# Optimization experiments

Hardware: AMD Instinct MI355X
Metric: run time of the kernel (lower is better)

Reference implementation:

```python
import jax, jax.numpy as jnp
import numpy as np

MU = 2.0 ** -10  # sign-LMS weight adaptation step


def setup_inputs() -> dict:
    key = jax.random.key(0)
    # 16-bit-range hyperspectral cube [Z, Y, X]
    image = jax.random.normal(key, (202, 256, 256), dtype=jnp.float32) * 1000.0
    # adaptive predictor weights per band over P=3 previous bands, init 0
    w0 = jnp.zeros((202, 3), dtype=jnp.float32)
    return {"image": image, "w0": w0}


def reference(image, w0):
    Z, Y, X = image.shape
    P = w0.shape[1]
    max_val = 2.0 ** 15 - 1.0  # dynamic_range = 16
    min_val = -(2.0 ** 15)

    # Spectral neighborhood: previous P bands at the same (y, x), zero-padded.
    # (lossless mode => sample representatives == original samples, so
    #  cross-band dependence uses raw samples directly)
    nb = jnp.stack(
        [jnp.pad(image, ((p + 1, 0), (0, 0), (0, 0)))[:Z] for p in range(P)],
        axis=-1,
    )  # [Z, Y, X, P]

    s_flat = image.reshape(Z, Y * X)       # BSQ raster order within each band
    nb_flat = nb.reshape(Z, Y * X, P)

    def band_scan(w_init, s_z, nb_z):
        # Sequential adaptive prediction within one band (strict data dependency)
        def step(w, inp):
            s, n = inp
            pred = jnp.clip(jnp.dot(w, n), min_val, max_val)
            res = s - pred
            w_new = w + MU * jnp.sign(res) * n  # sign-LMS update
            return w_new, (pred, res)

        _, (preds, ress) = jax.lax.scan(step, w_init, (s_z, nb_z))
        return preds, ress

    preds, ress = jax.vmap(band_scan)(w0, s_flat, nb_flat)  # bands independent
    predictions = preds.reshape(Z, Y, X)
    residuals = ress.reshape(Z, Y, X)

    # Lossless: quantized residual == residual; map rounded residual to
    # non-negative index delta = 2q (q>=0) or -2q-1 (q<0)
    q = jnp.round(residuals).astype(jnp.int32)
    mapped_indices = jnp.where(q >= 0, 2 * q, -2 * q - 1)
    quantized_residuals = residuals
    sample_representatives = image
    reconstructed = predictions + quantized_residuals

    return (predictions, residuals, quantized_residuals, mapped_indices,
            sample_representatives, reconstructed)
```

## Files before the change

kernel.cpp:

```cpp
#include <hip/hip_runtime.h>

#define ZB 202
#define ZBP 208
#define YX 65536
#define NTOT ((size_t)ZB * YX)

#define SS 128
#define NSS (YX / SS)
#define PAD 4

__device__ __forceinline__ constexpr float kMU() { return 0.0009765625f; }
#define MINV (-32768.0f)
#define MAXV (32767.0f)

typedef float v2f __attribute__((ext_vector_type(2)));

#define GL_LDS4(g, l)                                                     \
    __builtin_amdgcn_global_load_lds(                                     \
        (const __attribute__((address_space(1))) void*)(g),               \
        (__attribute__((address_space(3))) void*)(l), 4, 0, 0)

__global__ __launch_bounds__(256) void tr_kernel(const float* __restrict__ img,
                                                 float* __restrict__ imgT) {
    __shared__ float lds[64 * 65];
    const int t0 = blockIdx.x * 64;
    const int zi = blockIdx.y;
    const int zw0 = zi * 64 - 3;
    const int tid = threadIdx.x;
    const int c = tid & 63;
    const int r0 = tid >> 6;

    for (int k = 0; k < 16; ++k) {
        int rr = r0 * 16 + k;
        int z = zw0 + rr;
        float v = 0.0f;
        if (z >= 0 && z < ZB) v = img[(size_t)z * YX + t0 + c];
        lds[rr * 65 + c] = v;
    }
    __syncthreads();

    const int l = tid & 63;
    const int off = zi * 64 + l;
    if (off < ZBP) {
        for (int k = 0; k < 16; ++k) {
            int tr = r0 * 16 + k;
            imgT[(size_t)(t0 + tr) * ZBP + off] = lds[l * 65 + tr];
        }
    }
}

__global__ __launch_bounds__(512, 1) void scan_kernel(const float* __restrict__ imgT,
                                                      const float* __restrict__ w0g,
                                                      float* __restrict__ dT) {
    __shared__ float ldsf[PAD + 2 * SS * 64];

    const int tid = threadIdx.x;
    const int lane = tid & 63;
    const int wv = tid >> 6;
    const int b = blockIdx.x;
    const int goff = 61 * b + lane;
    const float* gsrc = imgT + goff;

    const int band = 61 * b + lane - 3;
    const bool live = (lane >= 3) && (band < ZB);
    const int wband = band < 0 ? 0 : (band > ZB - 1 ? ZB - 1 : band);
    float w0 = w0g[wband * 3 + 0];
    float w1 = w0g[wband * 3 + 1];
    float w2 = w0g[wband * 3 + 2];
    float* const sbase = live ? (dT + band) : (dT + NTOT + 70 + lane);

    auto stage = [&](int st) {
        float* lp = ldsf + PAD + (st & 1) * (SS * 64);
        const float* gp = gsrc + (size_t)st * (SS * ZBP);
        for (int r = wv - 1; r < SS; r += 7)
            GL_LDS4(gp + (size_t)r * ZBP, lp + r * 64);
    };

    v2f Aa[16], Ab[16], Ba[16], Bb[16];

#define RTISSUE(XA, XB, bsel, st_)                                             \
    {                                                                          \
        uint32_t a0_ = (uint32_t)(size_t)(__attribute__((address_space(3)))    \
            float*)(ldsf + (PAD + (bsel) * (SS * 64) + (st_) * (16 * 64)       \
                            + lane - 3));                                      \
        _Pragma("unroll") for (int k = 0; k < 16; ++k) {                       \
            uint32_t a_ = a0_ + (uint32_t)(k * 256);                           \
            asm volatile("ds_read2_b32 %0, %2 offset0:0 offset1:1\n\t"         \
                         "ds_read2_b32 %1, %2 offset0:2 offset1:3"             \
                         : "=&v"(XA[k]), "=&v"(XB[k])                          \
                         : "v"(a_));                                           \
        }                                                                      \
    }

#define KWAIT()                                                                \
    {                                                                          \
        asm volatile("s_waitcnt lgkmcnt(0)" ::: "memory");                     \
        __builtin_amdgcn_sched_barrier(0);                                     \
    }

#define CP(BA, BB, st_)                                                        \
    {                                                                          \
        float* op = sbase + ((size_t)ss * SS + (st_) * 16) * ZB;               \
        _Pragma("unroll") for (int i = 0; i < 16; ++i) {                       \
            const float nx = BA[i].x, ny = BA[i].y;                            \
            const float nz = BB[i].x, s_ = BB[i].y;                            \
            float d = __fadd_rn(                                               \
                __fadd_rn(__fmul_rn(w0, nz), __fmul_rn(w1, ny)),               \
                __fmul_rn(w2, nx));                                            \
            float sg = (s_ > d) ? kMU() : ((s_ < d) ? -kMU() : 0.0f);          \
            w0 = __builtin_fmaf(sg, nz, w0);                                   \
            w1 = __builtin_fmaf(sg, ny, w1);                                   \
            w2 = __builtin_fmaf(sg, nx, w2);                                   \
            op[(size_t)i * ZB] = d;                                            \
        }                                                                      \
    }

    if (wv != 0) stage(0);
    __syncthreads();

    for (int ss = 0; ss < NSS; ++ss) {
        if (wv != 0) {
            if (ss + 1 < NSS) stage(ss + 1);
        } else {
            const int csel = ss & 1;
            RTISSUE(Aa, Ab, csel, 0); KWAIT();
            RTISSUE(Ba, Bb, csel, 1); CP(Aa, Ab, 0); KWAIT();
            RTISSUE(Aa, Ab, csel, 2); CP(Ba, Bb, 1); KWAIT();
            RTISSUE(Ba, Bb, csel, 3); CP(Aa, Ab, 2); KWAIT();
            RTISSUE(Aa, Ab, csel, 4); CP(Ba, Bb, 3); KWAIT();
            RTISSUE(Ba, Bb, csel, 5); CP(Aa, Ab, 4); KWAIT();
            RTISSUE(Aa, Ab, csel, 6); CP(Ba, Bb, 5); KWAIT();
            RTISSUE(Ba, Bb, csel, 7); CP(Aa, Ab, 6); KWAIT();
            CP(Ba, Bb, 7);
        }
        __syncthreads();
    }

#undef RTISSUE
#undef KWAIT
#undef CP
}

__global__ __launch_bounds__(256) void finalize_kernel(const float* __restrict__ img,
                                                       const float* __restrict__ dT,
                                                       float* __restrict__ out) {
    __shared__ float lds[64 * ZB];
    const int t0 = blockIdx.x * 64;
    const float* src = dT + (size_t)t0 * ZB;
    for (int i = threadIdx.x; i < 64 * ZB; i += 256) lds[i] = src[i];
    __syncthreads();

    for (int k = 0; k < 51; ++k) {
        int e = k * 256 + threadIdx.x;
        if (e < 64 * ZB) {
            int zz = e >> 6;
            int tl = e & 63;
            float dv = lds[tl * ZB + zz];
            float pred = fminf(fmaxf(dv, MINV), MAXV);
            size_t o = (size_t)zz * YX + t0 + tl;
            float s = img[o];
            float res = __fsub_rn(s, pred);
            int q = (int)rintf(res);
            int m = (q >= 0) ? (2 * q) : (-2 * q - 1);
            out[o] = pred;
            out[NTOT + o] = res;
            out[2 * NTOT + o] = res;
            out[3 * NTOT + o] = (float)m;
            out[5 * NTOT + o] = __fadd_rn(pred, res);
        }
    }
}

__global__ __launch_bounds__(256) void repr_kernel(const float4* __restrict__ img4,
                                                   float4* __restrict__ out4) {
    size_t n4 = NTOT / 4;
    for (size_t i = (size_t)blockIdx.x * blockDim.x + threadIdx.x; i < n4;
         i += (size_t)gridDim.x * blockDim.x)
        out4[i] = img4[i];
}

extern "C" void kernel_launch(void* const* d_in, const int* in_sizes, int n_in,
                              void* d_out, int out_size, void* d_ws, size_t ws_size,
                              hipStream_t stream) {
    const float* img = (const float*)d_in[0];
    const float* w0g = (const float*)d_in[1];
    float* out = (float*)d_out;

    float* imgT = out;
    float* dT = out + 4 * NTOT;

    tr_kernel<<<dim3(YX / 64, 4), 256, 0, stream>>>(img, imgT);
    scan_kernel<<<4, 512, 0, stream>>>(imgT, w0g, dT);
    finalize_kernel<<<YX / 64, 256, 0, stream>>>(img, dT, out);
    repr_kernel<<<4096, 256, 0, stream>>>((const float4*)img, (float4*)(out + 4 * NTOT));
}
```

Measured before the change: 2.773 ms.

## Fuse transpose, finalize and copy into the scan kernel

The transpose, finalize and representative-copy kernels are removed. The scan kernel now gathers band data straight from the original image into LDS, writes predictions to an LDS output buffer, and its helper waves compute and store all six outputs for the previous chunk while wave 0 scans the current one. This avoids the transposed intermediate round trips through global memory and three extra launches. In exchange, all output traffic is issued by only 4 blocks (28 waves), and the LDS gathers use strided per-band 4-byte loads.

```diff
diff --git a/kernel.cpp b/kernel.cpp
--- a/kernel.cpp
+++ b/kernel.cpp
@@ -1,10 +1,9 @@
 #include <hip/hip_runtime.h>
+#include <stdint.h>
 
 #define ZB 202
-#define ZBP 208
 #define YX 65536
 #define NTOT ((size_t)ZB * YX)
-
 #define SS 128
 #define NSS (YX / SS)
 #define PAD 4
@@ -20,87 +19,115 @@
         (const __attribute__((address_space(1))) void*)(g),               \
         (__attribute__((address_space(3))) void*)(l), 4, 0, 0)
 
-__global__ __launch_bounds__(256) void tr_kernel(const float* __restrict__ img,
-                                                 float* __restrict__ imgT) {
-    __shared__ float lds[64 * 65];
-    const int t0 = blockIdx.x * 64;
-    const int zi = blockIdx.y;
-    const int zw0 = zi * 64 - 3;
-    const int tid = threadIdx.x;
-    const int c = tid & 63;
-    const int r0 = tid >> 6;
-
-    for (int k = 0; k < 16; ++k) {
-        int rr = r0 * 16 + k;
-        int z = zw0 + rr;
-        float v = 0.0f;
-        if (z >= 0 && z < ZB) v = img[(size_t)z * YX + t0 + c];
-        lds[rr * 65 + c] = v;
-    }
-    __syncthreads();
-
-    const int l = tid & 63;
-    const int off = zi * 64 + l;
-    if (off < ZBP) {
-        for (int k = 0; k < 16; ++k) {
-            int tr = r0 * 16 + k;
-            imgT[(size_t)(t0 + tr) * ZBP + off] = lds[l * 65 + tr];
-        }
-    }
-}
-
-__global__ __launch_bounds__(512, 1) void scan_kernel(const float* __restrict__ imgT,
+__global__ __launch_bounds__(512, 1) void scan_kernel(const float* __restrict__ img,
                                                       const float* __restrict__ w0g,
-                                                      float* __restrict__ dT) {
+                                                      float* __restrict__ out) {
     __shared__ float ldsf[PAD + 2 * SS * 64];
+    __shared__ float ldso[2 * SS * 64];
 
     const int tid = threadIdx.x;
     const int lane = tid & 63;
     const int wv = tid >> 6;
     const int b = blockIdx.x;
-    const int goff = 61 * b + lane;
-    const float* gsrc = imgT + goff;
+
+    float* const o_pred = out;
+    float* const o_res  = out + NTOT;
+    float* const o_qres = out + 2 * NTOT;
+    float* const o_map  = out + 3 * NTOT;
+    float* const o_repr = out + 4 * NTOT;
+    float* const o_rec  = out + 5 * NTOT;
 
     const int band = 61 * b + lane - 3;
-    const bool live = (lane >= 3) && (band < ZB);
     const int wband = band < 0 ? 0 : (band > ZB - 1 ? ZB - 1 : band);
     float w0 = w0g[wband * 3 + 0];
     float w1 = w0g[wband * 3 + 1];
     float w2 = w0g[wband * 3 + 2];
-    float* const sbase = live ? (dT + band) : (dT + NTOT + 70 + lane);
+    v2f Aa[16], Ab[16], Ba[16], Bb[16];
+    const uint32_t inb0 =
+        (uint32_t)(size_t)(__attribute__((address_space(3))) float*)(ldsf + PAD + lane - 3);
+    const uint32_t otbC =
+        (uint32_t)(size_t)(__attribute__((address_space(3))) float*)(ldso) + (uint32_t)(lane * 4);
+    const uint32_t otbP =
+        (uint32_t)(size_t)(__attribute__((address_space(3))) float*)(ldso) + (uint32_t)(lane * 256);
+
+    const int zcl = band < 0 ? 0 : (band > ZB - 1 ? ZB - 1 : band);
+    const float* const Bz = img + (size_t)zcl * YX;
+    const int cmax = (204 - 61 * b) < 63 ? (204 - 61 * b) : 63;
+
+    float sA[9], sB[9], dA[9], dB[9];
 
     auto stage = [&](int st) {
-        float* lp = ldsf + PAD + (st & 1) * (SS * 64);
-        const float* gp = gsrc + (size_t)st * (SS * ZBP);
+        float* lp0 = ldsf + PAD + (st & 1) * (SS * 64);
+        const float* p = Bz + (size_t)st * SS;
         for (int r = wv - 1; r < SS; r += 7)
-            GL_LDS4(gp + (size_t)r * ZBP, lp + r * 64);
+            GL_LDS4(p + r, lp0 + r * 64);
+    };
+    auto rezero = [&](int bn) {
+        float* lp0 = ldsf + PAD + bn * (SS * 64);
+        for (int r = wv - 1; r < SS; r += 7) {
+            lp0[r * 64 + 0] = 0.0f; lp0[r * 64 + 1] = 0.0f; lp0[r * 64 + 2] = 0.0f;
+        }
+    };
+    auto pissue = [&](int Tp, uint32_t pbuf) {
+#pragma unroll
+        for (int k = 0; k < 9; ++k) {
+            const int c = 2 + wv + 7 * k;
+            const int cc = c <= cmax ? c : 3;
+            const int zz = 61 * b + cc - 3;
+            const float* sp = img + (size_t)zz * YX + Tp + lane;
+            asm volatile("global_load_dword %0, %2, off\n\t"
+                         "global_load_dword %1, %2, off offset:256"
+                         : "=&v"(sA[k]), "=&v"(sB[k]) : "v"(sp));
+            uint32_t da = otbP + pbuf + (uint32_t)(cc * 4);
+            asm volatile("ds_read_b32 %0, %2\n\t"
+                         "ds_read_b32 %1, %2 offset:16384"
+                         : "=&v"(dA[k]), "=&v"(dB[k]) : "v"(da));
+        }
+    };
+    auto pstore = [&](int Tp) {
+#pragma unroll
+        for (int k = 0; k < 9; ++k) {
+            const int c = 2 + wv + 7 * k;
+            if (c > cmax) continue;
+            const int zz = 61 * b + c - 3;
+            const size_t o = (size_t)zz * YX + Tp + lane;
+#pragma unroll
+            for (int h = 0; h < 2; ++h) {
+                const float dv = h ? dB[k] : dA[k];
+                const float s = h ? sB[k] : sA[k];
+                const size_t oo = o + (size_t)(h * 64);
+                const float pred = fminf(fmaxf(dv, MINV), MAXV);
+                const float res = __fsub_rn(s, pred);
+                const int q = (int)rintf(res);
+                const int m = (q >= 0) ? (2 * q) : (-2 * q - 1);
+                o_pred[oo] = pred;
+                o_res[oo] = res;
+                o_qres[oo] = res;
+                o_map[oo] = (float)m;
+                o_repr[oo] = s;
+                o_rec[oo] = __fadd_rn(pred, res);
+            }
+        }
     };
 
-    v2f Aa[16], Ab[16], Ba[16], Bb[16];
-
-#define RTISSUE(XA, XB, bsel, st_)                                             \
+#define RTISSUE(XA, XB, cb_, st_)                                              \
     {                                                                          \
-        uint32_t a0_ = (uint32_t)(size_t)(__attribute__((address_space(3)))    \
-            float*)(ldsf + (PAD + (bsel) * (SS * 64) + (st_) * (16 * 64)       \
-                            + lane - 3));                                      \
+        uint32_t a0_ = inb0 + (cb_) + (uint32_t)((st_) * 4096);                \
         _Pragma("unroll") for (int k = 0; k < 16; ++k) {                       \
             uint32_t a_ = a0_ + (uint32_t)(k * 256);                           \
             asm volatile("ds_read2_b32 %0, %2 offset0:0 offset1:1\n\t"         \
                          "ds_read2_b32 %1, %2 offset0:2 offset1:3"             \
-                         : "=&v"(XA[k]), "=&v"(XB[k])                          \
-                         : "v"(a_));                                           \
+                         : "=&v"(XA[k]), "=&v"(XB[k]) : "v"(a_));              \
         }                                                                      \
     }
-
 #define KWAIT()                                                                \
     {                                                                          \
         asm volatile("s_waitcnt lgkmcnt(0)" ::: "memory");                     \
         __builtin_amdgcn_sched_barrier(0);                                     \
     }
-
-#define CP(BA, BB, st_)                                                        \
+#define CP(BA, BB, cb_, st_)                                                   \
     {                                                                          \
-        float* op = sbase + ((size_t)ss * SS + (st_) * 16) * ZB;               \
+        uint32_t ob_ = otbC + (cb_) + (uint32_t)((st_) * 4096);                \
         _Pragma("unroll") for (int i = 0; i < 16; ++i) {                       \
             const float nx = BA[i].x, ny = BA[i].y;                            \
             const float nz = BB[i].x, s_ = BB[i].y;                            \
@@ -111,72 +138,51 @@
             w0 = __builtin_fmaf(sg, nz, w0);                                   \
             w1 = __builtin_fmaf(sg, ny, w1);                                   \
             w2 = __builtin_fmaf(sg, nx, w2);                                   \
-            op[(size_t)i * ZB] = d;                                            \
+            asm volatile("ds_write_b32 %0, %1 offset:%c2"                      \
+                         :: "v"(ob_), "v"(d), "i"((i) * 256) : "memory");      \
         }                                                                      \
     }
 
-    if (wv != 0) stage(0);
+    if (wv != 0) {
+        stage(0);
+        asm volatile("s_waitcnt vmcnt(0)" ::: "memory");
+        if (b == 0) rezero(0);
+    }
     __syncthreads();
 
     for (int ss = 0; ss < NSS; ++ss) {
-        if (wv != 0) {
+        if (wv == 0) {
+            const uint32_t cb = (uint32_t)((ss & 1) * 32768);
+            RTISSUE(Aa, Ab, cb, 0); KWAIT();
+            RTISSUE(Ba, Bb, cb, 1); CP(Aa, Ab, cb, 0); KWAIT();
+            RTISSUE(Aa, Ab, cb, 2); CP(Ba, Bb, cb, 1); KWAIT();
+            RTISSUE(Ba, Bb, cb, 3); CP(Aa, Ab, cb, 2); KWAIT();
+            RTISSUE(Aa, Ab, cb, 4); CP(Ba, Bb, cb, 3); KWAIT();
+            RTISSUE(Ba, Bb, cb, 5); CP(Aa, Ab, cb, 4); KWAIT();
+            RTISSUE(Aa, Ab, cb, 6); CP(Ba, Bb, cb, 5); KWAIT();
+            RTISSUE(Ba, Bb, cb, 7); CP(Aa, Ab, cb, 6); KWAIT();
+            CP(Ba, Bb, cb, 7);
+        } else {
+            if (ss > 0) pissue((ss - 1) * SS, (uint32_t)(((ss - 1) & 1) * 32768));
             if (ss + 1 < NSS) stage(ss + 1);
-        } else {
-            const int csel = ss & 1;
-            RTISSUE(Aa, Ab, csel, 0); KWAIT();
-            RTISSUE(Ba, Bb, csel, 1); CP(Aa, Ab, 0); KWAIT();
-            RTISSUE(Aa, Ab, csel, 2); CP(Ba, Bb, 1); KWAIT();
-            RTISSUE(Ba, Bb, csel, 3); CP(Aa, Ab, 2); KWAIT();
-            RTISSUE(Aa, Ab, csel, 4); CP(Ba, Bb, 3); KWAIT();
-            RTISSUE(Ba, Bb, csel, 5); CP(Aa, Ab, 4); KWAIT();
-            RTISSUE(Aa, Ab, csel, 6); CP(Ba, Bb, 5); KWAIT();
-            RTISSUE(Ba, Bb, csel, 7); CP(Aa, Ab, 6); KWAIT();
-            CP(Ba, Bb, 7);
+            asm volatile("s_waitcnt vmcnt(0) lgkmcnt(0)" ::: "memory");
+            __builtin_amdgcn_sched_barrier(0);
+            if (ss > 0) pstore((ss - 1) * SS);
+            if (b == 0 && ss + 1 < NSS) rezero((ss + 1) & 1);
         }
         __syncthreads();
+    }
+
+    if (wv != 0) {
+        pissue((NSS - 1) * SS, (uint32_t)(((NSS - 1) & 1) * 32768));
+        asm volatile("s_waitcnt vmcnt(0) lgkmcnt(0)" ::: "memory");
+        __builtin_amdgcn_sched_barrier(0);
+        pstore((NSS - 1) * SS);
     }
 
 #undef RTISSUE
 #undef KWAIT
 #undef CP
-}
-
-__global__ __launch_bounds__(256) void finalize_kernel(const float* __restrict__ img,
-                                                       const float* __restrict__ dT,
-                                                       float* __restrict__ out) {
-    __shared__ float lds[64 * ZB];
-    const int t0 = blockIdx.x * 64;
-    const float* src = dT + (size_t)t0 * ZB;
-    for (int i = threadIdx.x; i < 64 * ZB; i += 256) lds[i] = src[i];
-    __syncthreads();
-
-    for (int k = 0; k < 51; ++k) {
-        int e = k * 256 + threadIdx.x;
-        if (e < 64 * ZB) {
-            int zz = e >> 6;
-            int tl = e & 63;
-            float dv = lds[tl * ZB + zz];
-            float pred = fminf(fmaxf(dv, MINV), MAXV);
-            size_t o = (size_t)zz * YX + t0 + tl;
-            float s = img[o];
-            float res = __fsub_rn(s, pred);
-            int q = (int)rintf(res);
-            int m = (q >= 0) ? (2 * q) : (-2 * q - 1);
-            out[o] = pred;
-            out[NTOT + o] = res;
-            out[2 * NTOT + o] = res;
-            out[3 * NTOT + o] = (float)m;
-            out[5 * NTOT + o] = __fadd_rn(pred, res);
-        }
-    }
-}
-
-__global__ __launch_bounds__(256) void repr_kernel(const float4* __restrict__ img4,
-                                                   float4* __restrict__ out4) {
-    size_t n4 = NTOT / 4;
-    for (size_t i = (size_t)blockIdx.x * blockDim.x + threadIdx.x; i < n4;
-         i += (size_t)gridDim.x * blockDim.x)
-        out4[i] = img4[i];
 }
 
 extern "C" void kernel_launch(void* const* d_in, const int* in_sizes, int n_in,
@@ -186,11 +192,5 @@
     const float* w0g = (const float*)d_in[1];
     float* out = (float*)d_out;
 
-    float* imgT = out;
-    float* dT = out + 4 * NTOT;
-
-    tr_kernel<<<dim3(YX / 64, 4), 256, 0, stream>>>(img, imgT);
-    scan_kernel<<<4, 512, 0, stream>>>(imgT, w0g, dT);
-    finalize_kernel<<<YX / 64, 256, 0, stream>>>(img, dT, out);
-    repr_kernel<<<4096, 256, 0, stream>>>((const float4*)img, (float4*)(out + 4 * NTOT));
+    scan_kernel<<<4, 512, 0, stream>>>(img, w0g, out);
 }
```

Measured after the change: 4.506 ms. 62.5% more time.
